# Performance work log

Measured on AMD Instinct MI355X. Metric: run time of the kernel, lower is better.

## Reference

```python
import jax, jax.numpy as jnp
import numpy as np

D, H, HK, DH = 2048, 32, 8, 64
RQ = RKV = 48
RO = RFF = 1024
INTER = 8192
B, T = 2, 1024
THETA = 10000.0
EPS = 1e-5
NEG = -1e30


def _rms(x, w):
    v = jnp.mean(x * x, axis=-1, keepdims=True)
    return x * jax.lax.rsqrt(v + EPS) * w


def _proj_per_head(x, Us, V):
    # x:[B,T,D], V:[h,r,D], Us:[h,dh,r] -> [B,h,T,dh]
    xr = jnp.einsum('btd,hrd->bthr', x, V)
    return jnp.einsum('bthr,hdr->bhtd', xr, Us)


def _rope_cos_sin(position_ids, dh):
    inv = 1.0 / (THETA ** (jnp.arange(0, dh, 2, dtype=jnp.float32) / dh))
    ang = position_ids.astype(jnp.float32)[:, None] * inv[None, :]   # [T, dh/2]
    ang = jnp.repeat(ang, 2, axis=-1)                                # interleaved, per source
    return jnp.cos(ang), jnp.sin(ang)                                # [T, dh]


def _rotate_half(x):
    d = x.shape[-1] // 2
    return jnp.concatenate([-x[..., d:], x[..., :d]], axis=-1)


def setup_inputs() -> dict:
    key = jax.random.key(0)
    ks = jax.random.split(key, 18)
    g = lambda i, shape, s: (jax.random.normal(ks[i], shape, jnp.float32) * s)
    return {
        'x': g(0, (B, T, D), 1.0),
        'position_ids': jnp.arange(T, dtype=jnp.int32),
        'ln1_w': jnp.ones((D,), jnp.float32),
        'ln2_w': jnp.ones((D,), jnp.float32),
        'q_Us': g(1, (H, DH, RQ), 0.05), 'q_V': g(2, (H, RQ, D), 0.05),
        'k_Us': g(3, (HK, DH, RKV), 0.05), 'k_V': g(4, (HK, RKV, D), 0.05),
        'v_Us': g(5, (HK, DH, RKV), 0.05), 'v_V': g(6, (HK, RKV, D), 0.05),
        'o_Us': g(7, (D, RO), 0.02), 'o_V': g(8, (RO, H * DH), 0.02),
        'g_Us': g(9, (INTER, RFF), 0.02), 'g_V': g(10, (RFF, D), 0.02),
        'u_Us': g(11, (INTER, RFF), 0.02), 'u_V': g(12, (RFF, D), 0.02),
        'd_Us': g(13, (D, RFF), 0.02), 'd_V': g(14, (RFF, INTER), 0.02),
    }


def reference(x, position_ids, ln1_w, ln2_w,
              q_Us, q_V, k_Us, k_V, v_Us, v_V,
              o_Us, o_V, g_Us, g_V, u_Us, u_V, d_Us, d_V):
    Bx, Tx, Dx = x.shape
    n_rep = H // HK

    # ---- attention sub-block ----
    h = _rms(x, ln1_w)
    q = _proj_per_head(h, q_Us, q_V)          # [B,H,T,dh]
    k = _proj_per_head(h, k_Us, k_V)          # [B,Hk,T,dh]
    v = _proj_per_head(h, v_Us, v_V)          # [B,Hk,T,dh]

    cos, sin = _rope_cos_sin(position_ids, DH)          # [T,dh]
    cos = cos[None, None]; sin = sin[None, None]
    q = q * cos + _rotate_half(q) * sin
    k = k * cos + _rotate_half(k) * sin

    k = jnp.repeat(k, n_rep, axis=1)          # GQA expand -> [B,H,T,dh]
    v = jnp.repeat(v, n_rep, axis=1)

    scale = 1.0 / jnp.sqrt(jnp.float32(DH))
    scores = jnp.einsum('bhtd,bhsd->bhts', q, k) * scale
    causal = jnp.tril(jnp.ones((Tx, Tx), bool))
    scores = jnp.where(causal[None, None], scores, NEG)
    p = jax.nn.softmax(scores, axis=-1)
    attn = jnp.einsum('bhts,bhsd->bhtd', p, v)            # [B,H,T,dh]
    attn = attn.transpose(0, 2, 1, 3).reshape(Bx, Tx, H * DH)

    # low-rank o projection: W_o ~= o_Us @ o_V
    ar = jnp.einsum('btk,rk->btr', attn, o_V)
    attn_out = jnp.einsum('btr,dr->btd', ar, o_Us)
    x = x + attn_out

    # ---- low-rank SwiGLU MLP ----
    h2 = _rms(x, ln2_w)
    gate = jnp.einsum('btr,ir->bti', jnp.einsum('btd,rd->btr', h2, g_V), g_Us)
    up = jnp.einsum('btr,ir->bti', jnp.einsum('btd,rd->btr', h2, u_V), u_Us)
    inner = jax.nn.silu(gate) * up
    down = jnp.einsum('btr,dr->btd', jnp.einsum('bti,ri->btr', inner, d_V), d_Us)
    return x + down
```

## Files before the change

kernel.cpp:

```cpp
#include <hip/hip_runtime.h>

typedef unsigned short u16;
typedef unsigned int u32;
typedef unsigned long long u64;

typedef __bf16 bf16x8 __attribute__((ext_vector_type(8)));
typedef float f32x4 __attribute__((ext_vector_type(4)));

__device__ __forceinline__ float bf2f(u16 u) {
  union { u32 i; float f; } v; v.i = ((u32)u) << 16; return v.f;
}
__device__ __forceinline__ u16 f2bf(float f) {
  union { float f; u32 i; } v; v.f = f;
  u32 r = v.i + 0x7fff + ((v.i >> 16) & 1);
  return (u16)(r >> 16);
}
__device__ __forceinline__ u32 packbf(float a, float b) {
  return (u32)f2bf(a) | ((u32)f2bf(b) << 16);
}

__device__ __forceinline__ void gload_lds16(const u16* g, u16* l) {
  __builtin_amdgcn_global_load_lds(
      (const __attribute__((address_space(1))) void*)g,
      (__attribute__((address_space(3))) void*)l, 16, 0, 0);
}

__global__ void detect_k(const u32* __restrict__ w, u32* __restrict__ flag) {
  if (threadIdx.x == 0 && blockIdx.x == 0)
    *flag = (w[0] == 0x3F803F80u) ? 0u : 1u;
}

struct CvtTab {
  const void* src[16];
  u64 doff[16];
  u32 bstart[16];
};

__global__ __launch_bounds__(256)
void convert_k(CvtTab tab, u16* __restrict__ wbase, const u32* __restrict__ dflag)
{
  const u32 f = *dflag;
  const int blk = blockIdx.x;
  int t = 15;
#pragma unroll
  for (int i = 15; i >= 1; i--) if (blk < (int)tab.bstart[i]) t = i - 1;
  const u64 eoff = (u64)(blk - tab.bstart[t]) * 2048 + threadIdx.x * 8;
  u16* dst = wbase + tab.doff[t] + eoff;
  if (f == 0) {
    uint4 v = *(const uint4*)((const u16*)tab.src[t] + eoff);
    *(uint4*)dst = v;
  } else {
    const float* s = (const float*)tab.src[t] + eoff;
    uint4 lo = *(const uint4*)s;
    uint4 hi = *(const uint4*)(s + 4);
    union { u32 i; float fv; } c0,c1,c2,c3,c4,c5,c6,c7;
    c0.i = lo.x; c1.i = lo.y; c2.i = lo.z; c3.i = lo.w;
    c4.i = hi.x; c5.i = hi.y; c6.i = hi.z; c7.i = hi.w;
    uint4 pb;
    pb.x = packbf(c0.fv, c1.fv); pb.y = packbf(c2.fv, c3.fv);
    pb.z = packbf(c4.fv, c5.fv); pb.w = packbf(c6.fv, c7.fv);
    *(uint4*)dst = pb;
  }
}

#define BKK 64

template<int EPI, int TILE>
__global__ __launch_bounds__(256)
void gemm_bt(const u16* __restrict__ A, const u16* __restrict__ B,
             void* Cout, const void* R,
             int K, int lda, int ldc, int pstride, const u32* __restrict__ dflag)
{
  constexpr int WT = TILE / 2;
  constexpr int NF = TILE / 32;
  constexpr int ITER = TILE / 32;
  __shared__ u16 sA[TILE * 64];
  __shared__ u16 sB[TILE * 64];
  const u32 f = *dflag;
  const int tid  = threadIdx.x;
  const int bm   = blockIdx.y * TILE;
  const int bn   = blockIdx.x * TILE;
  const int Klen = K / gridDim.z;
  const int kbase = blockIdx.z * Klen;
  const int wave = tid >> 6, lane = tid & 63;
  const int wm = (wave >> 1) * WT, wn = (wave & 1) * WT;
  const int lr = lane & 15, lq = lane >> 4;

  f32x4 acc[NF][NF];
#pragma unroll
  for (int i = 0; i < NF; i++)
#pragma unroll
    for (int j = 0; j < NF; j++) { f32x4 z = {0.f,0.f,0.f,0.f}; acc[i][j] = z; }

  int scA[ITER], scRow[ITER];
#pragma unroll
  for (int j = 0; j < ITER; j++) {
    int c = (wave * ITER + j) * 64 + lane;
    scRow[j] = c >> 3;
    scA[j] = ((c & 7) ^ (scRow[j] & 7)) * 8;
  }

  for (int k0 = kbase; k0 < kbase + Klen; k0 += BKK) {
#pragma unroll
    for (int j = 0; j < ITER; j++) {
      const u16* ga = A + (size_t)(bm + scRow[j]) * lda + k0 + scA[j];
      const u16* gb = B + (size_t)(bn + scRow[j]) * K + k0 + scA[j];
      gload_lds16(ga, &sA[(wave * ITER + j) * 512]);
      gload_lds16(gb, &sB[(wave * ITER + j) * 512]);
    }
    __syncthreads();
#pragma unroll
    for (int kk = 0; kk < BKK; kk += 32) {
      bf16x8 af[NF], bfr[NF];
#pragma unroll
      for (int i = 0; i < NF; i++)
        af[i] = *(const bf16x8*)
            &sA[(wm + i * 16 + lr) * 64 + ((((kk >> 3) + lq) ^ (lr & 7)) * 8)];
#pragma unroll
      for (int i = 0; i < NF; i++)
        bfr[i] = *(const bf16x8*)
            &sB[(wn + i * 16 + lr) * 64 + ((((kk >> 3) + lq) ^ (lr & 7)) * 8)];
#pragma unroll
      for (int i = 0; i < NF; i++)
#pragma unroll
        for (int j = 0; j < NF; j++)
          acc[i][j] = __builtin_amdgcn_mfma_f32_16x16x32_bf16(af[i], bfr[j], acc[i][j], 0, 0, 0);
    }
    __syncthreads();
  }

  u16* outz = (u16*)Cout + (size_t)blockIdx.z * pstride;
#pragma unroll
  for (int i = 0; i < NF; i++) {
#pragma unroll
    for (int j = 0; j < NF; j++) {
#pragma unroll
      for (int e = 0; e < 4; e++) {
        int row = bm + wm + i * 16 + lq * 4 + e;
        int col = bn + wn + j * 16 + lr;
        size_t idx = (size_t)row * ldc + col;
        float v = acc[i][j][e];
        if (EPI == 0) {
          outz[idx] = f2bf(v);
        } else if (EPI == 1) {
          float rv = f ? ((const float*)R)[idx] : bf2f(((const u16*)R)[idx]);
          ((float*)Cout)[idx] = v + rv;
        } else if (EPI == 2) {
          float s = v + ((const float*)R)[idx];
          if (f) ((float*)Cout)[idx] = s;
          else   ((u16*)Cout)[idx] = f2bf(s);
        } else {
          float g = bf2f(((const u16*)R)[idx]);
          float inner = g / (1.f + __expf(-g)) * v;
          ((u16*)Cout)[idx] = f2bf(inner);
        }
      }
    }
  }
}

__global__ __launch_bounds__(256)
void reduce2_k(const u16* __restrict__ p, u16* __restrict__ out, int nel)
{
  size_t i = ((size_t)blockIdx.x * 256 + threadIdx.x) * 8;
  uint4 a = *(const uint4*)(p + i);
  uint4 b = *(const uint4*)(p + (size_t)nel + i);
  u32 aa[4] = {a.x, a.y, a.z, a.w};
  u32 bb[4] = {b.x, b.y, b.z, b.w};
  u32 rr[4];
#pragma unroll
  for (int k = 0; k < 4; k++) {
    float s0 = bf2f((u16)aa[k]) + bf2f((u16)bb[k]);
    float s1 = bf2f((u16)(aa[k] >> 16)) + bf2f((u16)(bb[k] >> 16));
    rr[k] = packbf(s0, s1);
  }
  uint4 o; o.x = rr[0]; o.y = rr[1]; o.z = rr[2]; o.w = rr[3];
  *(uint4*)(out + i) = o;
}

template<int XSRC>
__global__ __launch_bounds__(256)
void rmsnorm_k(const void* __restrict__ xin, const u16* __restrict__ w,
               u16* __restrict__ out, const u32* __restrict__ dflag)
{
  const u32 f = *dflag;
  const int n = blockIdx.x, tid = threadIdx.x;
  float v[8]; float ss = 0.f;
#pragma unroll
  for (int i = 0; i < 8; i++) {
    int d = i * 256 + tid;
    float xv;
    if (XSRC == 1)      xv = ((const float*)xin)[(size_t)n * 2048 + d];
    else if (f)         xv = ((const float*)xin)[(size_t)n * 2048 + d];
    else                xv = bf2f(((const u16*)xin)[(size_t)n * 2048 + d]);
    v[i] = xv; ss += xv * xv;
  }
#pragma unroll
  for (int o = 32; o >= 1; o >>= 1) ss += __shfl_xor(ss, o, 64);
  __shared__ float red[4];
  if ((tid & 63) == 0) red[tid >> 6] = ss;
  __syncthreads();
  float tot = red[0] + red[1] + red[2] + red[3];
  float rms = rsqrtf(tot * (1.f / 2048.f) + 1e-5f);
#pragma unroll
  for (int i = 0; i < 8; i++) {
    int d = i * 256 + tid;
    out[(size_t)n * 2048 + d] = f2bf(v[i] * rms * bf2f(w[d]));
  }
}

template<int ROPE, int TRANS>
__global__ __launch_bounds__(256)
void qkv2_k(const u16* __restrict__ xr, const u16* __restrict__ Us,
            const int* __restrict__ pos, u16* __restrict__ out, int NH, int XS)
{
  const int h = blockIdx.y;
  const int tid = threadIdx.x;
  const int n = blockIdx.x * 8 + (tid >> 5);
  const int j = tid & 31;
  const u16* xrow = xr + (size_t)n * XS + h * 48;
  const u16* U = Us + (size_t)h * 64 * 48;
  float a = 0.f, b = 0.f;
#pragma unroll
  for (int r = 0; r < 48; r++) {
    float xv = bf2f(xrow[r]);
    a += xv * bf2f(U[j * 48 + r]);
    b += xv * bf2f(U[(j + 32) * 48 + r]);
  }
  const int t = n & 1023, bb = n >> 10;
  float olo, ohi;
  if (ROPE) {
    float p = (float)pos[t];
    float inv_lo = powf(10000.f, -(float)(2 * (j >> 1)) * (1.f / 64.f));
    float inv_hi = powf(10000.f, -(float)(2 * (16 + (j >> 1))) * (1.f / 64.f));
    float sl, cl, sh, ch;
    sincosf(p * inv_lo, &sl, &cl);
    sincosf(p * inv_hi, &sh, &ch);
    olo = a * cl - b * sl;
    ohi = b * ch + a * sh;
  } else { olo = a; ohi = b; }
  if (TRANS == 0) {
    size_t ob = ((size_t)(bb * NH + h) * 1024 + t) * 64;
    out[ob + j] = f2bf(olo);
    out[ob + j + 32] = f2bf(ohi);
  } else {
    size_t ob = (size_t)(bb * NH + h) * 64 * 1024;
    out[ob + (size_t)j * 1024 + t] = f2bf(olo);
    out[ob + (size_t)(j + 32) * 1024 + t] = f2bf(ohi);
  }
}

__global__ __launch_bounds__(256)
void flash_k(const u16* __restrict__ Q, const u16* __restrict__ K,
             const u16* __restrict__ VT, u16* __restrict__ O)
{
  __shared__ u16 sQ[64 * 72];
  __shared__ u16 sK[128 * 72];
  __shared__ u16 sVT[64 * 136];
  __shared__ u16 sP[64 * 136];
  const int bh = blockIdx.x;
  const int b = bh >> 5, h = bh & 31, hk = h >> 2;
  const int t0 = blockIdx.y << 6;
  const int tid = threadIdx.x, wave = tid >> 6, lane = tid & 63;
  const int lr = lane & 15, lq = lane >> 4;
  const int qr = wave * 16;
  const size_t bhk = (size_t)(b * 8 + hk);
  const u16* Qb = Q + ((size_t)bh * 1024 + t0) * 64;
  const u16* Kb = K + bhk * 1024 * 64;
  const u16* Vb = VT + bhk * 64 * 1024;

#pragma unroll
  for (int i = 0; i < 2; i++) {
    int c = tid + i * 256;
    int row = c >> 3, col = (c & 7) * 8;
    *(uint4*)&sQ[row * 72 + col] = *(const uint4*)(Qb + row * 64 + col);
  }

  f32x4 acc[4];
#pragma unroll
  for (int dt = 0; dt < 4; dt++) { f32x4 z = {0.f,0.f,0.f,0.f}; acc[dt] = z; }
  float m[4], l[4];
#pragma unroll
  for (int e = 0; e < 4; e++) { m[e] = -3.0e38f; l[e] = 0.f; }

  const int ntiles = (t0 >> 7) + 1;
  for (int st = 0; st < ntiles; st++) {
    __syncthreads();
#pragma unroll
    for (int i = 0; i < 4; i++) {
      int c = tid + i * 256;
      int row = c >> 3, col = (c & 7) * 8;
      *(uint4*)&sK[row * 72 + col] =
          *(const uint4*)(Kb + (size_t)(st * 128 + row) * 64 + col);
    }
#pragma unroll
    for (int i = 0; i < 4; i++) {
      int c = tid + i * 256;
      int d = c >> 4, t8 = (c & 15) * 8;
      *(uint4*)&sVT[d * 136 + t8] =
          *(const uint4*)(Vb + (size_t)d * 1024 + st * 128 + t8);
    }
    __syncthreads();

    bf16x8 aq0 = *(const bf16x8*)&sQ[(qr + lr) * 72 + lq * 8];
    bf16x8 aq1 = *(const bf16x8*)&sQ[(qr + lr) * 72 + 32 + lq * 8];
    f32x4 sf[8];
#pragma unroll
    for (int nt = 0; nt < 8; nt++) {
      f32x4 z = {0.f,0.f,0.f,0.f};
      bf16x8 bk0 = *(const bf16x8*)&sK[(nt * 16 + lr) * 72 + lq * 8];
      bf16x8 bk1 = *(const bf16x8*)&sK[(nt * 16 + lr) * 72 + 32 + lq * 8];
      z = __builtin_amdgcn_mfma_f32_16x16x32_bf16(aq0, bk0, z, 0, 0, 0);
      z = __builtin_amdgcn_mfma_f32_16x16x32_bf16(aq1, bk1, z, 0, 0, 0);
      sf[nt] = z;
    }

    const int colbase = st * 128;
#pragma unroll
    for (int e = 0; e < 4; e++) {
      const int row = t0 + qr + lq * 4 + e;
      float tm = -3.0e38f;
#pragma unroll
      for (int nt = 0; nt < 8; nt++) {
        float v = sf[nt][e] * 0.125f;
        if (colbase + nt * 16 + lr > row) v = -1e30f;
        sf[nt][e] = v;
        tm = fmaxf(tm, v);
      }
      tm = fmaxf(tm, __shfl_xor(tm, 1, 64));
      tm = fmaxf(tm, __shfl_xor(tm, 2, 64));
      tm = fmaxf(tm, __shfl_xor(tm, 4, 64));
      tm = fmaxf(tm, __shfl_xor(tm, 8, 64));
      float mnew = fmaxf(m[e], tm);
      float alpha = __expf(m[e] - mnew);
      m[e] = mnew;
      float ts = 0.f;
#pragma unroll
      for (int nt = 0; nt < 8; nt++) {
        float p = __expf(sf[nt][e] - mnew);
        sP[(qr + lq * 4 + e) * 136 + nt * 16 + lr] = f2bf(p);
        ts += p;
      }
      ts += __shfl_xor(ts, 1, 64);
      ts += __shfl_xor(ts, 2, 64);
      ts += __shfl_xor(ts, 4, 64);
      ts += __shfl_xor(ts, 8, 64);
      l[e] = l[e] * alpha + ts;
#pragma unroll
      for (int dt = 0; dt < 4; dt++) acc[dt][e] *= alpha;
    }

#pragma unroll
    for (int kk = 0; kk < 4; kk++) {
      bf16x8 pa = *(const bf16x8*)&sP[(qr + lr) * 136 + kk * 32 + lq * 8];
#pragma unroll
      for (int dt = 0; dt < 4; dt++) {
        bf16x8 bv = *(const bf16x8*)&sVT[(dt * 16 + lr) * 136 + kk * 32 + lq * 8];
        acc[dt] = __builtin_amdgcn_mfma_f32_16x16x32_bf16(pa, bv, acc[dt], 0, 0, 0);
      }
    }
  }

#pragma unroll
  for (int e = 0; e < 4; e++) {
    float inv = 1.f / l[e];
    int t = t0 + qr + lq * 4 + e;
#pragma unroll
    for (int dt = 0; dt < 4; dt++) {
      size_t idx = ((size_t)(b * 1024 + t)) * 2048 + h * 64 + dt * 16 + lr;
      O[idx] = f2bf(acc[dt][e] * inv);
    }
  }
}

extern "C" void kernel_launch(void* const* d_in, const int* in_sizes, int n_in,
                              void* d_out, int out_size, void* d_ws, size_t ws_size,
                              hipStream_t stream)
{
  const void* x    = d_in[0];
  const int* pos   = (const int*)d_in[1];

  char* ws = (char*)d_ws;
  const size_t MB = 1048576;
  float* x1     = (float*)(ws + 0 * MB);
  u16*   gate   = (u16*)  (ws + 16 * MB);
  u16*   h1     = (u16*)  (ws + 16 * MB);
  u16*   attn   = (u16*)  (ws + 16 * MB);
  u16*   xr_all = (u16*)  (ws + 24 * MB);
  u16*   ar     = (u16*)  (ws + 24 * MB);
  u16*   h2     = (u16*)  (ws + 28 * MB);
  u16*   qb     = (u16*)  (ws + 33 * MB);
  u16*   kb     = (u16*)  (ws + 41 * MB);
  u16*   vbt    = (u16*)  (ws + 43 * MB);
  u16*   part   = (u16*)  (ws + 48 * MB);
  u16*   gr_ur  = (u16*)  (ws + 48 * MB);
  u16*   dr     = (u16*)  (ws + 56 * MB);
  u16*   wb     = (u16*)  (ws + 60 * MB);
  u32*   flag   = (u32*)  (ws + 60 * MB + 81043456);

  u16* wQKV = wb + 0;
  u16* wGU  = wb + 4718592;
  u16* oVc  = wb + 8912896;
  u16* oUsc = wb + 11010048;
  u16* gUsc = wb + 13107200;
  u16* uUsc = wb + 21495808;
  u16* dVc  = wb + 29884416;
  u16* dUsc = wb + 38273024;
  u16* qUsc = wb + 40370176;
  u16* kUsc = wb + 40468480;
  u16* vUsc = wb + 40493056;
  u16* ln1c = wb + 40517632;
  u16* ln2c = wb + 40519680;

  CvtTab tab;
  const int srcidx[16] = {5, 7, 9, 13, 15, 11, 10, 12, 14, 17, 16, 4, 6, 8, 2, 3};
  const u64 doff[16] = {0, 3145728, 3932160, 4718592, 6815744, 8912896, 11010048,
                        13107200, 21495808, 29884416, 38273024, 40370176,
                        40468480, 40493056, 40517632, 40519680};
  const u32 bstart[16] = {0, 1536, 1920, 2304, 3328, 4352, 5376, 6400, 10496,
                          14592, 18688, 19712, 19760, 19772, 19784, 19785};
  for (int i = 0; i < 16; i++) {
    tab.src[i] = d_in[srcidx[i]];
    tab.doff[i] = doff[i];
    tab.bstart[i] = bstart[i];
  }

  dim3 blk(256);
  const int PS = 2097152;

  detect_k<<<1, 64, 0, stream>>>((const u32*)d_in[2], flag);
  convert_k<<<19786, blk, 0, stream>>>(tab, wb, flag);

  rmsnorm_k<0><<<2048, blk, 0, stream>>>(x, ln1c, h1, flag);

  gemm_bt<0,64><<<dim3(36, 32), blk, 0, stream>>>(h1, wQKV, xr_all, nullptr,
                                                  2048, 2048, 2304, 0, flag);

  qkv2_k<1,0><<<dim3(256, 32), blk, 0, stream>>>(xr_all,        qUsc, pos, qb, 32, 2304);
  qkv2_k<1,0><<<dim3(256, 8),  blk, 0, stream>>>(xr_all + 1536, kUsc, pos, kb, 8,  2304);
  qkv2_k<0,1><<<dim3(256, 8),  blk, 0, stream>>>(xr_all + 1920, vUsc, pos, vbt, 8, 2304);

  flash_k<<<dim3(64, 16), blk, 0, stream>>>(qb, kb, vbt, attn);

  gemm_bt<0,64><<<dim3(16, 32, 2), blk, 0, stream>>>(attn, oVc, part, nullptr,
                                                     2048, 2048, 1024, PS, flag);
  reduce2_k<<<1024, blk, 0, stream>>>(part, ar, PS);
  gemm_bt<1,64><<<dim3(32, 32), blk, 0, stream>>>(ar, oUsc, x1, x,
                                                  1024, 1024, 2048, 0, flag);

  rmsnorm_k<1><<<2048, blk, 0, stream>>>(x1, ln2c, h2, flag);

  gemm_bt<0,64><<<dim3(32, 32), blk, 0, stream>>>(h2, wGU, gr_ur, nullptr,
                                                  2048, 2048, 2048, 0, flag);
  gemm_bt<0,128><<<dim3(64, 16), blk, 0, stream>>>(gr_ur, gUsc, gate, nullptr,
                                                   1024, 2048, 8192, 0, flag);
  gemm_bt<3,128><<<dim3(64, 16), blk, 0, stream>>>(gr_ur + 1024, uUsc, gate, gate,
                                                   1024, 2048, 8192, 0, flag);

  gemm_bt<0,64><<<dim3(16, 32, 2), blk, 0, stream>>>(gate, dVc, part, nullptr,
                                                     8192, 8192, 1024, PS, flag);
  reduce2_k<<<1024, blk, 0, stream>>>(part, dr, PS);
  gemm_bt<2,64><<<dim3(32, 32), blk, 0, stream>>>(dr, dUsc, d_out, x1,
                                                  1024, 1024, 2048, 0, flag);
}
```

Baseline: 606.6 us.

## Fuse gate/up expansion GEMMs with SwiGLU epilogue and widen K tile

Replaces the two separate gate and up expansion GEMMs with one kernel that accumulates both products in registers and applies SiLU(gate)*up in the epilogue. This avoids writing and re-reading the large intermediate gate tensor. It also parameterises the K-tile depth and uses 128 for the smaller GEMMs to halve the number of barrier-separated iterations. The cost is more LDS per block and doubled accumulator registers in the fused kernel, which may reduce occupancy.

```diff
diff --git a/kernel.cpp b/kernel.cpp
--- a/kernel.cpp
+++ b/kernel.cpp
@@ -63,9 +63,7 @@
   }
 }
 
-#define BKK 64
-
-template<int EPI, int TILE>
+template<int EPI, int TILE, int BK>
 __global__ __launch_bounds__(256)
 void gemm_bt(const u16* __restrict__ A, const u16* __restrict__ B,
              void* Cout, const void* R,
@@ -73,9 +71,10 @@
 {
   constexpr int WT = TILE / 2;
   constexpr int NF = TILE / 32;
-  constexpr int ITER = TILE / 32;
-  __shared__ u16 sA[TILE * 64];
-  __shared__ u16 sB[TILE * 64];
+  constexpr int CH = BK / 8;
+  constexpr int ITER_S = TILE * CH / 256;
+  __shared__ u16 sA[TILE * BK];
+  __shared__ u16 sB[TILE * BK];
   const u32 f = *dflag;
   const int tid  = threadIdx.x;
   const int bm   = blockIdx.y * TILE;
@@ -92,34 +91,34 @@
 #pragma unroll
     for (int j = 0; j < NF; j++) { f32x4 z = {0.f,0.f,0.f,0.f}; acc[i][j] = z; }
 
-  int scA[ITER], scRow[ITER];
-#pragma unroll
-  for (int j = 0; j < ITER; j++) {
-    int c = (wave * ITER + j) * 64 + lane;
-    scRow[j] = c >> 3;
-    scA[j] = ((c & 7) ^ (scRow[j] & 7)) * 8;
-  }
-
-  for (int k0 = kbase; k0 < kbase + Klen; k0 += BKK) {
-#pragma unroll
-    for (int j = 0; j < ITER; j++) {
+  int scA[ITER_S], scRow[ITER_S];
+#pragma unroll
+  for (int j = 0; j < ITER_S; j++) {
+    int s = (wave * ITER_S + j) * 64 + lane;
+    scRow[j] = s / CH;
+    scA[j] = (((s % CH)) ^ (scRow[j] & 7)) * 8;
+  }
+
+  for (int k0 = kbase; k0 < kbase + Klen; k0 += BK) {
+#pragma unroll
+    for (int j = 0; j < ITER_S; j++) {
       const u16* ga = A + (size_t)(bm + scRow[j]) * lda + k0 + scA[j];
       const u16* gb = B + (size_t)(bn + scRow[j]) * K + k0 + scA[j];
-      gload_lds16(ga, &sA[(wave * ITER + j) * 512]);
-      gload_lds16(gb, &sB[(wave * ITER + j) * 512]);
+      gload_lds16(ga, &sA[(wave * ITER_S + j) * 512]);
+      gload_lds16(gb, &sB[(wave * ITER_S + j) * 512]);
     }
     __syncthreads();
 #pragma unroll
-    for (int kk = 0; kk < BKK; kk += 32) {
+    for (int kk = 0; kk < BK; kk += 32) {
       bf16x8 af[NF], bfr[NF];
 #pragma unroll
       for (int i = 0; i < NF; i++)
         af[i] = *(const bf16x8*)
-            &sA[(wm + i * 16 + lr) * 64 + ((((kk >> 3) + lq) ^ (lr & 7)) * 8)];
+            &sA[(wm + i * 16 + lr) * BK + ((((kk >> 3) + lq) ^ (lr & 7)) * 8)];
 #pragma unroll
       for (int i = 0; i < NF; i++)
         bfr[i] = *(const bf16x8*)
-            &sB[(wn + i * 16 + lr) * 64 + ((((kk >> 3) + lq) ^ (lr & 7)) * 8)];
+            &sB[(wn + i * 16 + lr) * BK + ((((kk >> 3) + lq) ^ (lr & 7)) * 8)];
 #pragma unroll
       for (int i = 0; i < NF; i++)
 #pragma unroll
@@ -149,11 +148,96 @@
           float s = v + ((const float*)R)[idx];
           if (f) ((float*)Cout)[idx] = s;
           else   ((u16*)Cout)[idx] = f2bf(s);
+        }
+      }
+    }
+  }
+}
+
+__global__ __launch_bounds__(256)
+void gemm_gu(const u16* __restrict__ A, const u16* __restrict__ Bg,
+             const u16* __restrict__ Bu, u16* __restrict__ Cout,
+             int K, int lda, int ldc)
+{
+  constexpr int TILE = 128, BK = 64, NF = 4, CH = 8, ITER_S = 4;
+  __shared__ u16 sA[TILE * BK];
+  __shared__ u16 sB[TILE * BK];
+  const int tid  = threadIdx.x;
+  const int bm   = blockIdx.y * TILE;
+  const int bn   = blockIdx.x * TILE;
+  const int wave = tid >> 6, lane = tid & 63;
+  const int wm = (wave >> 1) * 64, wn = (wave & 1) * 64;
+  const int lr = lane & 15, lq = lane >> 4;
+
+  f32x4 accG[NF][NF], accU[NF][NF];
+#pragma unroll
+  for (int i = 0; i < NF; i++)
+#pragma unroll
+    for (int j = 0; j < NF; j++) {
+      f32x4 z = {0.f,0.f,0.f,0.f}; accG[i][j] = z; accU[i][j] = z;
+    }
+
+  int scA[ITER_S], scRow[ITER_S];
+#pragma unroll
+  for (int j = 0; j < ITER_S; j++) {
+    int s = (wave * ITER_S + j) * 64 + lane;
+    scRow[j] = s / CH;
+    scA[j] = ((s % CH) ^ (scRow[j] & 7)) * 8;
+  }
+
+#pragma unroll
+  for (int ph = 0; ph < 2; ph++) {
+    const u16* Ap = A + (ph ? 1024 : 0);
+    const u16* Bp = ph ? Bu : Bg;
+    for (int k0 = 0; k0 < K; k0 += BK) {
+#pragma unroll
+      for (int j = 0; j < ITER_S; j++) {
+        gload_lds16(Ap + (size_t)(bm + scRow[j]) * lda + k0 + scA[j],
+                    &sA[(wave * ITER_S + j) * 512]);
+        gload_lds16(Bp + (size_t)(bn + scRow[j]) * K + k0 + scA[j],
+                    &sB[(wave * ITER_S + j) * 512]);
+      }
+      __syncthreads();
+#pragma unroll
+      for (int kk = 0; kk < BK; kk += 32) {
+        bf16x8 af[NF], bfr[NF];
+#pragma unroll
+        for (int i = 0; i < NF; i++)
+          af[i] = *(const bf16x8*)
+              &sA[(wm + i * 16 + lr) * BK + ((((kk >> 3) + lq) ^ (lr & 7)) * 8)];
+#pragma unroll
+        for (int i = 0; i < NF; i++)
+          bfr[i] = *(const bf16x8*)
+              &sB[(wn + i * 16 + lr) * BK + ((((kk >> 3) + lq) ^ (lr & 7)) * 8)];
+        if (ph == 0) {
+#pragma unroll
+          for (int i = 0; i < NF; i++)
+#pragma unroll
+            for (int j = 0; j < NF; j++)
+              accG[i][j] = __builtin_amdgcn_mfma_f32_16x16x32_bf16(af[i], bfr[j], accG[i][j], 0, 0, 0);
         } else {
-          float g = bf2f(((const u16*)R)[idx]);
-          float inner = g / (1.f + __expf(-g)) * v;
-          ((u16*)Cout)[idx] = f2bf(inner);
+#pragma unroll
+          for (int i = 0; i < NF; i++)
+#pragma unroll
+            for (int j = 0; j < NF; j++)
+              accU[i][j] = __builtin_amdgcn_mfma_f32_16x16x32_bf16(af[i], bfr[j], accU[i][j], 0, 0, 0);
         }
+      }
+      __syncthreads();
+    }
+  }
+
+#pragma unroll
+  for (int i = 0; i < NF; i++) {
+#pragma unroll
+    for (int j = 0; j < NF; j++) {
+#pragma unroll
+      for (int e = 0; e < 4; e++) {
+        int row = bm + wm + i * 16 + lq * 4 + e;
+        int col = bn + wn + j * 16 + lr;
+        float g = accG[i][j][e];
+        float inner = g / (1.f + __expf(-g)) * accU[i][j][e];
+        Cout[(size_t)row * ldc + col] = f2bf(inner);
       }
     }
   }
@@ -433,8 +517,8 @@
 
   rmsnorm_k<0><<<2048, blk, 0, stream>>>(x, ln1c, h1, flag);
 
-  gemm_bt<0,64><<<dim3(36, 32), blk, 0, stream>>>(h1, wQKV, xr_all, nullptr,
-                                                  2048, 2048, 2304, 0, flag);
+  gemm_bt<0,64,128><<<dim3(36, 32), blk, 0, stream>>>(h1, wQKV, xr_all, nullptr,
+                                                      2048, 2048, 2304, 0, flag);
 
   qkv2_k<1,0><<<dim3(256, 32), blk, 0, stream>>>(xr_all,        qUsc, pos, qb, 32, 2304);
   qkv2_k<1,0><<<dim3(256, 8),  blk, 0, stream>>>(xr_all + 1536, kUsc, pos, kb, 8,  2304);
@@ -442,24 +526,23 @@
 
   flash_k<<<dim3(64, 16), blk, 0, stream>>>(qb, kb, vbt, attn);
 
-  gemm_bt<0,64><<<dim3(16, 32, 2), blk, 0, stream>>>(attn, oVc, part, nullptr,
-                                                     2048, 2048, 1024, PS, flag);
+  gemm_bt<0,64,128><<<dim3(16, 32, 2), blk, 0, stream>>>(attn, oVc, part, nullptr,
+                                                         2048, 2048, 1024, PS, flag);
   reduce2_k<<<1024, blk, 0, stream>>>(part, ar, PS);
-  gemm_bt<1,64><<<dim3(32, 32), blk, 0, stream>>>(ar, oUsc, x1, x,
-                                                  1024, 1024, 2048, 0, flag);
+  gemm_bt<1,64,128><<<dim3(32, 32), blk, 0, stream>>>(ar, oUsc, x1, x,
+                                                      1024, 1024, 2048, 0, flag);
 
   rmsnorm_k<1><<<2048, blk, 0, stream>>>(x1, ln2c, h2, flag);
 
-  gemm_bt<0,64><<<dim3(32, 32), blk, 0, stream>>>(h2, wGU, gr_ur, nullptr,
-                                                  2048, 2048, 2048, 0, flag);
-  gemm_bt<0,128><<<dim3(64, 16), blk, 0, stream>>>(gr_ur, gUsc, gate, nullptr,
-                                                   1024, 2048, 8192, 0, flag);
-  gemm_bt<3,128><<<dim3(64, 16), blk, 0, stream>>>(gr_ur + 1024, uUsc, gate, gate,
-                                                   1024, 2048, 8192, 0, flag);
-
-  gemm_bt<0,64><<<dim3(16, 32, 2), blk, 0, stream>>>(gate, dVc, part, nullptr,
-                                                     8192, 8192, 1024, PS, flag);
+  gemm_bt<0,64,128><<<dim3(32, 32), blk, 0, stream>>>(h2, wGU, gr_ur, nullptr,
+                                                      2048, 2048, 2048, 0, flag);
+
+  gemm_gu<<<dim3(64, 16), blk, 0, stream>>>(gr_ur, gUsc, uUsc, gate,
+                                            1024, 2048, 8192);
+
+  gemm_bt<0,64,128><<<dim3(16, 32, 2), blk, 0, stream>>>(gate, dVc, part, nullptr,
+                                                         8192, 8192, 1024, PS, flag);
   reduce2_k<<<1024, blk, 0, stream>>>(part, dr, PS);
-  gemm_bt<2,64><<<dim3(32, 32), blk, 0, stream>>>(dr, dUsc, d_out, x1,
-                                                  1024, 1024, 2048, 0, flag);
-}
+  gemm_bt<2,64,128><<<dim3(32, 32), blk, 0, stream>>>(dr, dUsc, d_out, x1,
+                                                      1024, 1024, 2048, 0, flag);
+}
```

Result: faster. 589.1 us (-2.9%).
